# Kernel optimization log

Measured on AMD Instinct MI355X. Metric: run time of the kernel, lower is better.

The kernel has to match this reference:

```python
import jax, jax.numpy as jnp
import numpy as np

N, E, G = 50000, 600000, 50
IN_CH, HID, OUT, HEADS = 5, 64, 32, 4
BN_EPS = 1e-5


def setup_inputs() -> dict:
    key = jax.random.key(0)
    ks = jax.random.split(key, 32)

    def p(i, shape, scale=0.1):
        return jax.random.normal(ks[i], shape, dtype=jnp.float32) * scale

    inp = {
        "x": jax.random.normal(ks[0], (N, IN_CH), dtype=jnp.float32),
        "edge_index": jax.random.randint(ks[1], (2, E), 0, N),
        "batch": jnp.sort(jax.random.randint(ks[2], (N,), 0, G)),
        "enc_w": p(3, (IN_CH, HID)),
        "enc_b": jnp.zeros((HID,), jnp.float32),
    }
    dims = [(HID, HID), (HID, HID), (HID, OUT)]
    i = 4
    for l, (din, dout) in enumerate(dims):
        inp[f"w{l}"] = p(i, (din, HEADS * dout)); i += 1
        inp[f"as{l}"] = p(i, (HEADS, dout)); i += 1
        inp[f"ad{l}"] = p(i, (HEADS, dout)); i += 1
        inp[f"b{l}"] = jnp.zeros((dout,), jnp.float32)
        inp[f"g{l}"] = jnp.ones((dout,), jnp.float32)
        inp[f"be{l}"] = jnp.zeros((dout,), jnp.float32)
    for name in ("eth", "man"):
        inp[f"{name}_w1"] = p(i, (OUT, OUT // 2)); i += 1
        inp[f"{name}_b1"] = jnp.zeros((OUT // 2,), jnp.float32)
        inp[f"{name}_w2"] = p(i, (OUT // 2, 1)); i += 1
        inp[f"{name}_b2"] = jnp.zeros((1,), jnp.float32)
    return inp


def _gat(h_in, src, dst, W, a_s, a_d, bias, dout):
    # PyG GATConv, heads=HEADS, concat=False (mean over heads)
    h = (h_in @ W).reshape(N, HEADS, dout)          # [N,H,C]
    es = (h * a_s).sum(-1)                          # [N,H] src attention term
    ed = (h * a_d).sum(-1)                          # [N,H] dst attention term
    e = jax.nn.leaky_relu(es[src] + ed[dst], 0.2)   # [E,H]
    m = jax.ops.segment_max(e, dst, num_segments=N)
    ex = jnp.exp(e - m[dst])
    s = jax.ops.segment_sum(ex, dst, num_segments=N)
    alpha = ex / (s[dst] + 1e-16)                   # edge softmax per dst
    out = jax.ops.segment_sum(h[src] * alpha[..., None], dst, num_segments=N)
    return out.mean(axis=1) + bias                  # mean over heads + bias


def _bn(x, g, b):  # BatchNorm1d with batch statistics
    mu = x.mean(0)
    var = x.var(0)
    return g * (x - mu) * jax.lax.rsqrt(var + BN_EPS) + b


def _head(g, w1, b1, w2, b2):
    return jax.nn.sigmoid(jax.nn.relu(g @ w1 + b1) @ w2 + b2)


def reference(x, edge_index, batch, enc_w, enc_b,
              w0, as0, ad0, b0, g0, be0,
              w1, as1, ad1, b1, g1, be1,
              w2, as2, ad2, b2, g2, be2,
              eth_w1, eth_b1, eth_w2, eth_b2,
              man_w1, man_b1, man_w2, man_b2):
    loops = jnp.arange(N)
    src = jnp.concatenate([edge_index[0], loops])
    dst = jnp.concatenate([edge_index[1], loops])

    h = x @ enc_w + enc_b
    layers = [(w0, as0, ad0, b0, g0, be0, HID),
              (w1, as1, ad1, b1, g1, be1, HID),
              (w2, as2, ad2, b2, g2, be2, OUT)]
    for i, (W, a_s, a_d, bias, gm, bt, dout) in enumerate(layers):
        h = _gat(h, src, dst, W, a_s, a_d, bias, dout)
        h = _bn(h, gm, bt)
        if i < len(layers) - 1:
            h = jax.nn.relu(h)  # dropout is identity at inference

    ones = jnp.ones((N,), h.dtype)
    counts = jax.ops.segment_sum(ones, batch, num_segments=G)  # [G]
    gsum = jax.ops.segment_sum(h, batch, num_segments=G)
    gmean = gsum / jnp.maximum(counts, 1.0)[:, None]
    gmax = jax.ops.segment_max(h, batch, num_segments=G)
    gmax = jnp.where(counts[:, None] > 0, gmax, 0.0)
    gemb = (gmean + gmax + gsum) / 3.0

    ethics = _head(gemb, eth_w1, eth_b1, eth_w2, eth_b2)
    manip = _head(gemb, man_w1, man_b1, man_w2, man_b2)
    return h, gemb, ethics, manip
```

## Files before the change

### kernel.cpp

```cpp
#include <hip/hip_runtime.h>
#include <math.h>

constexpr int kN  = 50000;
constexpr int kE  = 600000;
constexpr int kET = 650000;
constexpr int kG  = 50;
constexpr int kH  = 4;
constexpr int kRep = 16;
constexpr int kRangeSz = 6250;

constexpr size_t OFF_HCUR   = 0;
constexpr size_t OFF_HNEXT  = 1600000;
constexpr size_t OFF_Z      = 4800000;
constexpr size_t OFF_ES     = 11200000;
constexpr size_t OFF_ED     = 11400000;
constexpr size_t OFF_ROWPTR = 14200000;
constexpr size_t OFF_SRC    = 14320000;
constexpr size_t OFF_WT2    = 14970000;
constexpr size_t OFF_AHAT   = 15000000;
constexpr size_t OFF_SPART  = 15002000;
constexpr size_t OFF_CURSOR = 15010000;
constexpr size_t OFF_BNREP  = 15060000;
constexpr size_t OFF_GPOOL  = 15066144;
constexpr size_t kZeroEnd   = 15069344;

constexpr int kScanBlocks = (kN + 1023) / 1024;
constexpr int kHistBlocks = (kET + 255) / 256;
constexpr int kPrepBlocks = 163;
constexpr int kEncBlocks  = kN / 4;
constexpr int kChunks     = (kE + 1023) / 1024;
constexpr int kSctBlocks  = kChunks * 8;
constexpr int kLoopBlocks = (kN + 255) / 256;

typedef __bf16 bf16x8 __attribute__((ext_vector_type(8)));
typedef float  f32x4  __attribute__((ext_vector_type(4)));

__device__ inline ushort f2b(float f) {
    unsigned u = __float_as_uint(f);
    return (ushort)((u + 0x7FFFu + ((u >> 16) & 1u)) >> 16);
}
__device__ inline float b2f(ushort u) {
    return __uint_as_float(((unsigned)u) << 16);
}
__device__ inline unsigned enc_f(float f) {
    unsigned b = __float_as_uint(f);
    return (b & 0x80000000u) ? ~b : (b | 0x80000000u);
}
__device__ inline float dec_f(unsigned u) {
    return __uint_as_float((u & 0x80000000u) ? (u & 0x7FFFFFFFu) : ~u);
}

__device__ inline void edge_pair(const int* __restrict__ ei, int e, int& src, int& dst) {
    if (e < kE) { src = ei[e]; dst = ei[kE + e]; }
    else        { src = e - kE; dst = e - kE; }
}

__global__ void k_histprep(const int* __restrict__ ei, int* __restrict__ counts,
                           const float* __restrict__ w0, const float* __restrict__ w1,
                           const float* __restrict__ w2, const float* __restrict__ as0,
                           const float* __restrict__ as1, const float* __restrict__ as2,
                           const float* __restrict__ ad0, const float* __restrict__ ad1,
                           const float* __restrict__ ad2, float* __restrict__ ahat,
                           ushort* __restrict__ Wt2) {
    int b = blockIdx.x;
    if (b < 3) {
        const float* W  = (b == 0) ? w0 : (b == 1) ? w1 : w2;
        const float* As = (b == 0) ? as0 : (b == 1) ? as1 : as2;
        const float* Ad = (b == 0) ? ad0 : (b == 1) ? ad1 : ad2;
        int dout = (b == 2) ? 32 : 64;
        int i = threadIdx.x;
        int h = i >> 6, k = i & 63;
        const float* wr = W + (size_t)k * (4 * dout) + h * dout;
        float s1 = 0.f, s2 = 0.f;
        for (int c = 0; c < dout; ++c) {
            float w = wr[c];
            s1 += w * As[h * dout + c];
            s2 += w * Ad[h * dout + c];
        }
        ahat[b * 512 + i] = s1;
        ahat[b * 512 + 256 + i] = s2;
    } else if (b < kPrepBlocks) {
        int i = (b - 3) * 256 + threadIdx.x;
        if (i >= 40960) return;
        int l, li;
        if (i < 16384)      { l = 0; li = i; }
        else if (i < 32768) { l = 1; li = i - 16384; }
        else                { l = 2; li = i - 32768; }
        int dout = (l == 2) ? 32 : 64;
        const float* W = (l == 0) ? w0 : (l == 1) ? w1 : w2;
        int c = li >> 8, kk = li & 255;
        int h = kk >> 6, k = kk & 63;
        Wt2[l * 16384 + li] = f2b(W[(size_t)k * (4 * dout) + h * dout + c]);
    } else {
        int e = (b - kPrepBlocks) * 256 + threadIdx.x;
        if (e >= kET) return;
        int src, dst;
        edge_pair(ei, e, src, dst);
        atomicAdd(&counts[dst], 1);
    }
}

__global__ void __launch_bounds__(1024) k_scan_local(const int* __restrict__ counts,
                                                     int* __restrict__ rowptr,
                                                     int* __restrict__ partials) {
    int tid = threadIdx.x;
    int idx = blockIdx.x * 1024 + tid;
    int val = (idx < kN) ? counts[idx] : 0;
    int lane = tid & 63, w = tid >> 6;
    int x = val;
#pragma unroll
    for (int off = 1; off < 64; off <<= 1) {
        int t = __shfl_up(x, off);
        if (lane >= off) x += t;
    }
    __shared__ int wsum[16];
    if (lane == 63) wsum[w] = x;
    __syncthreads();
    if (w == 0 && lane < 16) {
        int y = wsum[lane];
#pragma unroll
        for (int off = 1; off < 16; off <<= 1) {
            int t = __shfl_up(y, off);
            if (lane >= off) y += t;
        }
        wsum[lane] = y;
    }
    __syncthreads();
    int incl = x + (w > 0 ? wsum[w - 1] : 0);
    if (idx < kN) rowptr[idx + 1] = incl;
    if (tid == 1023) partials[blockIdx.x] = incl;
}

__global__ void k_scan_part(int* __restrict__ partials) {
    int lane = threadIdx.x;
    int v = (lane < kScanBlocks) ? partials[lane] : 0;
    int x = v;
#pragma unroll
    for (int off = 1; off < 64; off <<= 1) {
        int t = __shfl_up(x, off);
        if (lane >= off) x += t;
    }
    if (lane < kScanBlocks) partials[lane] = x - v;
}

__global__ void __launch_bounds__(1024) k_scan_add(int* __restrict__ cursor,
                                                   int* __restrict__ rowptr,
                                                   const int* __restrict__ partials) {
    int idx = blockIdx.x * 1024 + threadIdx.x;
    if (idx >= kN) return;
    int incl = rowptr[idx + 1] + partials[blockIdx.x];
    rowptr[idx + 1] = incl;
    int val = cursor[idx];
    cursor[idx] = incl - val;
    if (idx == 0) rowptr[0] = 0;
}

__global__ void __launch_bounds__(256) k_scatter_enc(const int* __restrict__ ei,
                                                     int* __restrict__ cursor,
                                                     ushort* __restrict__ src_csr,
                                                     const int* __restrict__ rowptr,
                                                     const float* __restrict__ x,
                                                     const float* __restrict__ w,
                                                     const float* __restrict__ b,
                                                     const float* __restrict__ ahat0,
                                                     ushort* __restrict__ h,
                                                     float* __restrict__ es,
                                                     float* __restrict__ ed) {
    if (blockIdx.x < kEncBlocks) {
        int node = blockIdx.x * 4 + (threadIdx.x >> 6);
        int lane = threadIdx.x & 63;
        float acc = b[lane];
#pragma unroll
        for (int k = 0; k < 5; ++k) acc += x[node * 5 + k] * w[k * 64 + lane];
        h[(size_t)node * 64 + lane] = f2b(acc);

        float ps[4], pd[4];
#pragma unroll
        for (int hh = 0; hh < 4; ++hh) {
            ps[hh] = acc * ahat0[hh * 64 + lane];
            pd[hh] = acc * ahat0[256 + hh * 64 + lane];
        }
#pragma unroll
        for (int off = 1; off < 64; off <<= 1) {
#pragma unroll
            for (int hh = 0; hh < 4; ++hh) {
                ps[hh] += __shfl_xor(ps[hh], off);
                pd[hh] += __shfl_xor(pd[hh], off);
            }
        }
        if (lane == 0) {
            ((float4*)es)[node] = make_float4(ps[0], ps[1], ps[2], ps[3]);
            ((float4*)ed)[node] = make_float4(pd[0], pd[1], pd[2], pd[3]);
        }
    } else if (blockIdx.x < kEncBlocks + kSctBlocks) {
        int bs = blockIdx.x - kEncBlocks;
        int chunk = bs >> 3;
        int range = blockIdx.x & 7;
        int dlo = range * kRangeSz;
        int e0 = (chunk * 256 + threadIdx.x) * 4;
        if (e0 >= kE) return;
        int4 dv = *reinterpret_cast<const int4*>(ei + kE + e0);
        int4 sv = *reinterpret_cast<const int4*>(ei + e0);
        int dstv[4] = {dv.x, dv.y, dv.z, dv.w};
        int srcv[4] = {sv.x, sv.y, sv.z, sv.w};
#pragma unroll
        for (int u = 0; u < 4; ++u) {
            if (e0 + u < kE && (unsigned)(dstv[u] - dlo) < (unsigned)kRangeSz) {
                int pos = atomicAdd(&cursor[dstv[u]], 1);
                src_csr[pos] = (ushort)srcv[u];
            }
        }
    } else {
        int d = (blockIdx.x - kEncBlocks - kSctBlocks) * 256 + threadIdx.x;
        if (d >= kN) return;
        src_csr[rowptr[d + 1] - 1] = (ushort)d;
    }
}

__global__ void __launch_bounds__(256) k_gat(const int* __restrict__ rowptr,
                                             const ushort* __restrict__ srcc,
                                             const float* __restrict__ es,
                                             const float* __restrict__ ed,
                                             const ushort* __restrict__ h,
                                             ushort* __restrict__ z) {
    int wid = threadIdx.x >> 6;
    int lane = threadIdx.x & 63;
    int dst = blockIdx.x * 4 + wid;
    int start = rowptr[dst], end = rowptr[dst + 1];
    int deg = end - start;

    int e_l = lane >> 2, hh = lane & 3;
    int q = lane >> 4, c4 = lane & 15;

    float edv = ed[dst * 4 + hh];
    float acc[4][4] = {};
    float s;

    if (deg <= 16) {
        int pos = start + e_l;
        int psafe = (pos < end) ? pos : start;
        int src = srcc[psafe];
        float v = es[src * 4 + hh] + edv;
        v = (v >= 0.f) ? v : 0.2f * v;
        if (pos >= end) v = -3e38f;

        uint2 hv[4];
#pragma unroll
        for (int t = 0; t < 4; ++t) {
            int p2 = start + t * 4 + q;
            int p2s = (p2 < end) ? p2 : start;
            int s2 = srcc[p2s];
            hv[t] = *reinterpret_cast<const uint2*>(h + (size_t)s2 * 64 + c4 * 4);
        }

        float cm = v;
        cm = fmaxf(cm, __shfl_xor(cm, 4));
        cm = fmaxf(cm, __shfl_xor(cm, 8));
        cm = fmaxf(cm, __shfl_xor(cm, 16));
        cm = fmaxf(cm, __shfl_xor(cm, 32));
        float p = __expf(v - cm);
        float cs = p;
        cs += __shfl_xor(cs, 4);
        cs += __shfl_xor(cs, 8);
        cs += __shfl_xor(cs, 16);
        cs += __shfl_xor(cs, 32);
        s = cs;

#pragma unroll
        for (int t = 0; t < 4; ++t) {
            int el = t * 4 + q;
            float p0 = __shfl(p, (el << 2) | 0);
            float p1 = __shfl(p, (el << 2) | 1);
            float p2 = __shfl(p, (el << 2) | 2);
            float p3 = __shfl(p, (el << 2) | 3);
            float c0 = __uint_as_float(hv[t].x << 16);
            float c1 = __uint_as_float(hv[t].x & 0xFFFF0000u);
            float c2 = __uint_as_float(hv[t].y << 16);
            float c3 = __uint_as_float(hv[t].y & 0xFFFF0000u);
            acc[0][0] += p0 * c0; acc[0][1] += p0 * c1; acc[0][2] += p0 * c2; acc[0][3] += p0 * c3;
            acc[1][0] += p1 * c0; acc[1][1] += p1 * c1; acc[1][2] += p1 * c2; acc[1][3] += p1 * c3;
            acc[2][0] += p2 * c0; acc[2][1] += p2 * c1; acc[2][2] += p2 * c2; acc[2][3] += p2 * c3;
            acc[3][0] += p3 * c0; acc[3][1] += p3 * c1; acc[3][2] += p3 * c2; acc[3][3] += p3 * c3;
        }
    } else {
        float m = -3e38f;
        s = 0.f;
        for (int cs0 = start; cs0 < end; cs0 += 16) {
            int pos = cs0 + e_l;
            int psafe = (pos < end) ? pos : start;
            int src = srcc[psafe];
            float v = es[src * 4 + hh] + edv;
            v = (v >= 0.f) ? v : 0.2f * v;
            if (pos >= end) v = -3e38f;

            float cm = v;
            cm = fmaxf(cm, __shfl_xor(cm, 4));
            cm = fmaxf(cm, __shfl_xor(cm, 8));
            cm = fmaxf(cm, __shfl_xor(cm, 16));
            cm = fmaxf(cm, __shfl_xor(cm, 32));
            float mn = fmaxf(m, cm);
            float scale = __expf(m - mn);
            float p = __expf(v - mn);
            float cth = p;
            cth += __shfl_xor(cth, 4);
            cth += __shfl_xor(cth, 8);
            cth += __shfl_xor(cth, 16);
            cth += __shfl_xor(cth, 32);
            s = s * scale + cth;
            m = mn;

            float sc0 = __shfl(scale, 0), sc1 = __shfl(scale, 1);
            float sc2 = __shfl(scale, 2), sc3 = __shfl(scale, 3);
#pragma unroll
            for (int c = 0; c < 4; ++c) {
                acc[0][c] *= sc0; acc[1][c] *= sc1; acc[2][c] *= sc2; acc[3][c] *= sc3;
            }
#pragma unroll
            for (int t = 0; t < 4; ++t) {
                int el = t * 4 + q;
                int p2 = cs0 + el;
                int p2s = (p2 < end) ? p2 : start;
                int s2 = srcc[p2s];
                uint2 hv = *reinterpret_cast<const uint2*>(h + (size_t)s2 * 64 + c4 * 4);
                float p0 = __shfl(p, (el << 2) | 0);
                float p1 = __shfl(p, (el << 2) | 1);
                float p2f = __shfl(p, (el << 2) | 2);
                float p3 = __shfl(p, (el << 2) | 3);
                float c0 = __uint_as_float(hv.x << 16);
                float c1 = __uint_as_float(hv.x & 0xFFFF0000u);
                float c2 = __uint_as_float(hv.y << 16);
                float c3 = __uint_as_float(hv.y & 0xFFFF0000u);
                acc[0][0] += p0 * c0;  acc[0][1] += p0 * c1;  acc[0][2] += p0 * c2;  acc[0][3] += p0 * c3;
                acc[1][0] += p1 * c0;  acc[1][1] += p1 * c1;  acc[1][2] += p1 * c2;  acc[1][3] += p1 * c3;
                acc[2][0] += p2f * c0; acc[2][1] += p2f * c1; acc[2][2] += p2f * c2; acc[2][3] += p2f * c3;
                acc[3][0] += p3 * c0;  acc[3][1] += p3 * c1;  acc[3][2] += p3 * c2;  acc[3][3] += p3 * c3;
            }
        }
    }

    float myinv = 0.25f / (s + 1e-16f);
    float inv0 = __shfl(myinv, 0), inv1 = __shfl(myinv, 1);
    float inv2 = __shfl(myinv, 2), inv3 = __shfl(myinv, 3);
#pragma unroll
    for (int c = 0; c < 4; ++c) {
        acc[0][c] *= inv0; acc[1][c] *= inv1; acc[2][c] *= inv2; acc[3][c] *= inv3;
    }
#pragma unroll
    for (int j = 0; j < 4; ++j) {
#pragma unroll
        for (int c = 0; c < 4; ++c) {
            float v = acc[j][c];
            v += __shfl_xor(v, 16);
            v += __shfl_xor(v, 32);
            acc[j][c] = v;
        }
    }
    if (q == 0) {
        ushort* zr = z + (size_t)dst * 256 + c4 * 4;
#pragma unroll
        for (int j = 0; j < 4; ++j) {
            ushort4 o;
            o.x = f2b(acc[j][0]); o.y = f2b(acc[j][1]);
            o.z = f2b(acc[j][2]); o.w = f2b(acc[j][3]);
            *reinterpret_cast<ushort4*>(zr + j * 64) = o;
        }
    }
}

template <int DOUT>
__global__ void __launch_bounds__(256) k_zgemm(const ushort* __restrict__ z,
                                               const ushort* __restrict__ Wt2l,
                                               float* __restrict__ hnext,
                                               float* __restrict__ bnrep_l) {
    constexpr int NT = DOUT / 16;
    constexpr int W = 2 * DOUT;
    __shared__ float pl[4][W];
    int tid = threadIdx.x;
    int widx = tid >> 6, lane = tid & 63;
    int wid = blockIdx.x * 4 + widx;
    int mtile = wid / NT;
    int nt = wid - mtile * NT;
    bool active = (mtile < kN / 16);
    int m0 = mtile * 16;
    int n0 = nt * 16;

    int row = lane & 15;
    int k0  = (lane >> 4) * 8;

    for (int j = tid; j < 4 * W; j += 256) (&pl[0][0])[j] = 0.f;

    f32x4 acc = {0.f, 0.f, 0.f, 0.f};
    if (active) {
        const ushort* za = z + (size_t)(m0 + row) * 256 + k0;
        const ushort* wb = Wt2l + (size_t)(n0 + row) * 256 + k0;
#pragma unroll
        for (int ks = 0; ks < 8; ++ks) {
            bf16x8 a = *reinterpret_cast<const bf16x8*>(za + ks * 32);
            bf16x8 b = *reinterpret_cast<const bf16x8*>(wb + ks * 32);
            acc = __builtin_amdgcn_mfma_f32_16x16x32_bf16(a, b, acc, 0, 0, 0);
        }
        int col = lane & 15;
        int r0  = (lane >> 4) * 4;
#pragma unroll
        for (int r = 0; r < 4; ++r)
            hnext[(size_t)(m0 + r0 + r) * DOUT + n0 + col] = acc[r];
    }

    float s0 = 0.f, q0 = 0.f;
#pragma unroll
    for (int r = 0; r < 4; ++r) { s0 += acc[r]; q0 += acc[r] * acc[r]; }
    s0 += __shfl_xor(s0, 16); s0 += __shfl_xor(s0, 32);
    q0 += __shfl_xor(q0, 16); q0 += __shfl_xor(q0, 32);
    __syncthreads();
    if (lane < 16) {
        pl[widx][n0 + lane]        = s0;
        pl[widx][DOUT + n0 + lane] = q0;
    }
    __syncthreads();
    if (tid < W) {
        float t = pl[0][tid] + pl[1][tid] + pl[2][tid] + pl[3][tid];
        atomicAdd(&bnrep_l[(blockIdx.x & (kRep - 1)) * 128 + tid], t);
    }
}

__global__ void __launch_bounds__(256) k_bn_apply_att(const float* __restrict__ hnext,
                                                      const float* __restrict__ bnrep_l,
                                                      const float* __restrict__ g,
                                                      const float* __restrict__ be,
                                                      const float* __restrict__ ahat_next,
                                                      ushort* __restrict__ hcur,
                                                      float* __restrict__ es,
                                                      float* __restrict__ ed) {
    int node = blockIdx.x * 4 + (threadIdx.x >> 6);
    int lane = threadIdx.x & 63;
    float bs = 0.f, bq = 0.f;
#pragma unroll
    for (int r = 0; r < kRep; ++r) {
        bs += bnrep_l[r * 128 + lane];
        bq += bnrep_l[r * 128 + 64 + lane];
    }
    float mu = bs * (1.f / kN);
    float var = bq * (1.f / kN) - mu * mu;
    float v = g[lane] * (hnext[(size_t)node * 64 + lane] - mu) * rsqrtf(var + 1e-5f) + be[lane];
    v = fmaxf(v, 0.f);
    hcur[(size_t)node * 64 + lane] = f2b(v);

    float ps[4], pd[4];
#pragma unroll
    for (int hh = 0; hh < 4; ++hh) {
        ps[hh] = v * ahat_next[hh * 64 + lane];
        pd[hh] = v * ahat_next[256 + hh * 64 + lane];
    }
#pragma unroll
    for (int off = 1; off < 64; off <<= 1) {
#pragma unroll
        for (int hh = 0; hh < 4; ++hh) {
            ps[hh] += __shfl_xor(ps[hh], off);
            pd[hh] += __shfl_xor(pd[hh], off);
        }
    }
    if (lane == 0) {
        ((float4*)es)[node] = make_float4(ps[0], ps[1], ps[2], ps[3]);
        ((float4*)ed)[node] = make_float4(pd[0], pd[1], pd[2], pd[3]);
    }
}

__global__ void __launch_bounds__(256) k_bn_apply32_pool(const float* __restrict__ hnext,
                                                         const float* __restrict__ bnrep_l,
                                                         const float* __restrict__ g,
                                                         const float* __restrict__ be,
                                                         const int* __restrict__ batch,
                                                         float* __restrict__ out_h,
                                                         float* __restrict__ gsum,
                                                         unsigned* __restrict__ gmaxe) {
    int tid = threadIdx.x;
    int i = blockIdx.x * 256 + tid;
    int n = i >> 5, c = i & 31;
    float bs = 0.f, bq = 0.f;
#pragma unroll
    for (int r = 0; r < kRep; ++r) {
        bs += bnrep_l[r * 128 + c];
        bq += bnrep_l[r * 128 + 32 + c];
    }
    float mu = bs * (1.f / kN);
    float var = bq * (1.f / kN) - mu * mu;
    float v = g[c] * (hnext[i] - mu) * rsqrtf(var + 1e-5f) + be[c];
    out_h[i] = v;

    __shared__ float ls[256];
    ls[tid] = v;
    __syncthreads();
    int nb0 = blockIdx.x * 8;
    int gfirst = batch[nb0], glast = batch[nb0 + 7];
    if (gfirst == glast) {
        if (tid < 32) {
            float s = 0.f;
            unsigned me = 0u;
#pragma unroll
            for (int r = 0; r < 8; ++r) {
                float vv = ls[r * 32 + tid];
                s += vv;
                unsigned e = enc_f(vv);
                me = (e > me) ? e : me;
            }
            atomicAdd(&gsum[gfirst * 32 + tid], s);
            atomicMax(&gmaxe[gfirst * 32 + tid], me);
        }
    } else {
        int gg = batch[n];
        atomicAdd(&gsum[gg * 32 + c], v);
        atomicMax(&gmaxe[gg * 32 + c], enc_f(v));
    }
}

__global__ void __launch_bounds__(256) k_finish(const float* __restrict__ gsum,
                                                const unsigned* __restrict__ gmaxe,
                                                const int* __restrict__ batch,
                                                const float* __restrict__ ew1,
                                                const float* __restrict__ eb1,
                                                const float* __restrict__ ew2,
                                                const float* __restrict__ eb2,
                                                const float* __restrict__ mw1,
                                                const float* __restrict__ mb1,
                                                const float* __restrict__ mw2,
                                                const float* __restrict__ mb2,
                                                float* __restrict__ out_gemb,
                                                float* __restrict__ out_eth,
                                                float* __restrict__ out_man) {
    __shared__ int bound[kG + 1];
    __shared__ float ge[kG * 32];
    int tid = threadIdx.x;
    if (tid <= kG) {
        int lo = 0, hi = kN;
        while (lo < hi) { int mid = (lo + hi) >> 1; if (batch[mid] < tid) lo = mid + 1; else hi = mid; }
        bound[tid] = lo;
    }
    __syncthreads();
    for (int j = tid; j < kG * 32; j += 256) {
        int gg = j >> 5;
        int cnt = bound[gg + 1] - bound[gg];
        float sum = gsum[j];
        float mx = (cnt > 0) ? dec_f(gmaxe[j]) : 0.f;
        float mean = sum / fmaxf((float)cnt, 1.f);
        float e = (mean + mx + sum) * (1.f / 3.f);
        ge[j] = e;
        out_gemb[j] = e;
    }
    __syncthreads();
    if (tid < kG) {
        const float* row = &ge[tid * 32];
        float acc_e = eb2[0], acc_m = mb2[0];
#pragma unroll 4
        for (int j = 0; j < 16; ++j) {
            float he = eb1[j], hm = mb1[j];
            for (int k = 0; k < 32; ++k) {
                float v = row[k];
                he += v * ew1[k * 16 + j];
                hm += v * mw1[k * 16 + j];
            }
            acc_e += fmaxf(he, 0.f) * ew2[j];
            acc_m += fmaxf(hm, 0.f) * mw2[j];
        }
        out_eth[tid] = 1.f / (1.f + expf(-acc_e));
        out_man[tid] = 1.f / (1.f + expf(-acc_m));
    }
}

extern "C" void kernel_launch(void* const* d_in, const int* in_sizes, int n_in,
                              void* d_out, int out_size, void* d_ws, size_t ws_size,
                              hipStream_t stream) {
    const float* x     = (const float*)d_in[0];
    const int*   ei    = (const int*)d_in[1];
    const int*   batch = (const int*)d_in[2];
    const float* enc_w = (const float*)d_in[3];
    const float* enc_b = (const float*)d_in[4];

    float* ws = (float*)d_ws;
    ushort*   hcur  = (ushort*)(ws + OFF_HCUR);
    float*    hnext = ws + OFF_HNEXT;
    ushort*   z     = (ushort*)(ws + OFF_Z);
    float*    es    = ws + OFF_ES;
    float*    ed    = ws + OFF_ED;
    int*      rowptr= (int*)(ws + OFF_ROWPTR);
    ushort*   srcc  = (ushort*)(ws + OFF_SRC);
    ushort*   Wt2   = (ushort*)(ws + OFF_WT2);
    float*    ahat  = ws + OFF_AHAT;
    int*      spart = (int*)(ws + OFF_SPART);
    int*      cursor= (int*)(ws + OFF_CURSOR);
    float*    bnrep = ws + OFF_BNREP;
    float*    gsum  = ws + OFF_GPOOL;
    unsigned* gmaxe = (unsigned*)(ws + OFF_GPOOL + 1600);

    float* out      = (float*)d_out;
    float* out_h    = out;
    float* out_gemb = out + 1600000;
    float* out_eth  = out + 1601600;
    float* out_man  = out + 1601650;

    hipMemsetAsync(ws + OFF_CURSOR, 0, (kZeroEnd - OFF_CURSOR) * sizeof(float), stream);

    k_histprep<<<kPrepBlocks + kHistBlocks, 256, 0, stream>>>(
        ei, cursor,
        (const float*)d_in[5], (const float*)d_in[11], (const float*)d_in[17],
        (const float*)d_in[6], (const float*)d_in[12], (const float*)d_in[18],
        (const float*)d_in[7], (const float*)d_in[13], (const float*)d_in[19],
        ahat, Wt2);

    k_scan_local<<<kScanBlocks, 1024, 0, stream>>>(cursor, rowptr, spart);
    k_scan_part<<<1, 64, 0, stream>>>(spart);
    k_scan_add<<<kScanBlocks, 1024, 0, stream>>>(cursor, rowptr, spart);

    k_scatter_enc<<<kEncBlocks + kSctBlocks + kLoopBlocks, 256, 0, stream>>>(
        ei, cursor, srcc, rowptr, x, enc_w, enc_b, ahat, hcur, es, ed);

    for (int l = 0; l < 3; ++l) {
        const float* gam = (const float*)d_in[9 + 6 * l];
        const float* bet = (const float*)d_in[10 + 6 * l];
        const ushort* Wt2l = Wt2 + l * 16384;
        float* bnrep_l = bnrep + l * kRep * 128;

        k_gat<<<kN / 4, 256, 0, stream>>>(rowptr, srcc, es, ed, hcur, z);

        if (l < 2) {
            k_zgemm<64><<<3125, 256, 0, stream>>>(z, Wt2l, hnext, bnrep_l);
            k_bn_apply_att<<<kN / 4, 256, 0, stream>>>(hnext, bnrep_l, gam, bet,
                                                       ahat + (l + 1) * 512, hcur, es, ed);
        } else {
            k_zgemm<32><<<1563, 256, 0, stream>>>(z, Wt2l, hnext, bnrep_l);
            k_bn_apply32_pool<<<kN * 32 / 256, 256, 0, stream>>>(hnext, bnrep_l, gam, bet,
                                                                 batch, out_h, gsum, gmaxe);
        }
    }

    k_finish<<<1, 256, 0, stream>>>(gsum, gmaxe, batch,
                                    (const float*)d_in[23], (const float*)d_in[24],
                                    (const float*)d_in[25], (const float*)d_in[26],
                                    (const float*)d_in[27], (const float*)d_in[28],
                                    (const float*)d_in[29], (const float*)d_in[30],
                                    out_gemb, out_eth, out_man);
}
```

Measured before the change: 473.7 us.

## Restructure GAT aggregation to one channel per lane with LDS-shared attention weights

The GAT aggregation kernel drops its separate low-degree path and its cross-quarter shuffle reduction. Each lane now owns one of the 64 channels and loops serially over the edges in a chunk. Softmax weights and rescale factors are passed through per-wave shared memory instead of shuffles. This removes many shuffles and the final reduction, but gathers of h become 2-byte scalar loads done one edge at a time. That means more sequential memory latency per destination, and the shared-memory exchange relies on the wave running in lockstep with no barrier.

```diff
diff --git a/kernel.cpp b/kernel.cpp
--- a/kernel.cpp
+++ b/kernel.cpp
@@ -223,148 +223,70 @@
                                              const float* __restrict__ ed,
                                              const ushort* __restrict__ h,
                                              ushort* __restrict__ z) {
+    __shared__ float pls[4][72];
     int wid = threadIdx.x >> 6;
     int lane = threadIdx.x & 63;
     int dst = blockIdx.x * 4 + wid;
     int start = rowptr[dst], end = rowptr[dst + 1];
-    int deg = end - start;
 
     int e_l = lane >> 2, hh = lane & 3;
-    int q = lane >> 4, c4 = lane & 15;
+    int c = lane;
 
     float edv = ed[dst * 4 + hh];
-    float acc[4][4] = {};
-    float s;
-
-    if (deg <= 16) {
-        int pos = start + e_l;
+    float acc0 = 0.f, acc1 = 0.f, acc2 = 0.f, acc3 = 0.f;
+    float m = -3e38f, s = 0.f;
+    float* pw = pls[wid];
+
+    for (int cs0 = start; cs0 < end; cs0 += 16) {
+        int pos = cs0 + e_l;
         int psafe = (pos < end) ? pos : start;
         int src = srcc[psafe];
         float v = es[src * 4 + hh] + edv;
         v = (v >= 0.f) ? v : 0.2f * v;
         if (pos >= end) v = -3e38f;
 
-        uint2 hv[4];
-#pragma unroll
-        for (int t = 0; t < 4; ++t) {
-            int p2 = start + t * 4 + q;
-            int p2s = (p2 < end) ? p2 : start;
-            int s2 = srcc[p2s];
-            hv[t] = *reinterpret_cast<const uint2*>(h + (size_t)s2 * 64 + c4 * 4);
-        }
-
         float cm = v;
         cm = fmaxf(cm, __shfl_xor(cm, 4));
         cm = fmaxf(cm, __shfl_xor(cm, 8));
         cm = fmaxf(cm, __shfl_xor(cm, 16));
         cm = fmaxf(cm, __shfl_xor(cm, 32));
-        float p = __expf(v - cm);
-        float cs = p;
-        cs += __shfl_xor(cs, 4);
-        cs += __shfl_xor(cs, 8);
-        cs += __shfl_xor(cs, 16);
-        cs += __shfl_xor(cs, 32);
-        s = cs;
-
-#pragma unroll
-        for (int t = 0; t < 4; ++t) {
-            int el = t * 4 + q;
-            float p0 = __shfl(p, (el << 2) | 0);
-            float p1 = __shfl(p, (el << 2) | 1);
-            float p2 = __shfl(p, (el << 2) | 2);
-            float p3 = __shfl(p, (el << 2) | 3);
-            float c0 = __uint_as_float(hv[t].x << 16);
-            float c1 = __uint_as_float(hv[t].x & 0xFFFF0000u);
-            float c2 = __uint_as_float(hv[t].y << 16);
-            float c3 = __uint_as_float(hv[t].y & 0xFFFF0000u);
-            acc[0][0] += p0 * c0; acc[0][1] += p0 * c1; acc[0][2] += p0 * c2; acc[0][3] += p0 * c3;
-            acc[1][0] += p1 * c0; acc[1][1] += p1 * c1; acc[1][2] += p1 * c2; acc[1][3] += p1 * c3;
-            acc[2][0] += p2 * c0; acc[2][1] += p2 * c1; acc[2][2] += p2 * c2; acc[2][3] += p2 * c3;
-            acc[3][0] += p3 * c0; acc[3][1] += p3 * c1; acc[3][2] += p3 * c2; acc[3][3] += p3 * c3;
-        }
-    } else {
-        float m = -3e38f;
-        s = 0.f;
-        for (int cs0 = start; cs0 < end; cs0 += 16) {
-            int pos = cs0 + e_l;
-            int psafe = (pos < end) ? pos : start;
-            int src = srcc[psafe];
-            float v = es[src * 4 + hh] + edv;
-            v = (v >= 0.f) ? v : 0.2f * v;
-            if (pos >= end) v = -3e38f;
-
-            float cm = v;
-            cm = fmaxf(cm, __shfl_xor(cm, 4));
-            cm = fmaxf(cm, __shfl_xor(cm, 8));
-            cm = fmaxf(cm, __shfl_xor(cm, 16));
-            cm = fmaxf(cm, __shfl_xor(cm, 32));
-            float mn = fmaxf(m, cm);
-            float scale = __expf(m - mn);
-            float p = __expf(v - mn);
-            float cth = p;
-            cth += __shfl_xor(cth, 4);
-            cth += __shfl_xor(cth, 8);
-            cth += __shfl_xor(cth, 16);
-            cth += __shfl_xor(cth, 32);
-            s = s * scale + cth;
-            m = mn;
-
-            float sc0 = __shfl(scale, 0), sc1 = __shfl(scale, 1);
-            float sc2 = __shfl(scale, 2), sc3 = __shfl(scale, 3);
-#pragma unroll
-            for (int c = 0; c < 4; ++c) {
-                acc[0][c] *= sc0; acc[1][c] *= sc1; acc[2][c] *= sc2; acc[3][c] *= sc3;
-            }
-#pragma unroll
-            for (int t = 0; t < 4; ++t) {
-                int el = t * 4 + q;
-                int p2 = cs0 + el;
-                int p2s = (p2 < end) ? p2 : start;
-                int s2 = srcc[p2s];
-                uint2 hv = *reinterpret_cast<const uint2*>(h + (size_t)s2 * 64 + c4 * 4);
-                float p0 = __shfl(p, (el << 2) | 0);
-                float p1 = __shfl(p, (el << 2) | 1);
-                float p2f = __shfl(p, (el << 2) | 2);
-                float p3 = __shfl(p, (el << 2) | 3);
-                float c0 = __uint_as_float(hv.x << 16);
-                float c1 = __uint_as_float(hv.x & 0xFFFF0000u);
-                float c2 = __uint_as_float(hv.y << 16);
-                float c3 = __uint_as_float(hv.y & 0xFFFF0000u);
-                acc[0][0] += p0 * c0;  acc[0][1] += p0 * c1;  acc[0][2] += p0 * c2;  acc[0][3] += p0 * c3;
-                acc[1][0] += p1 * c0;  acc[1][1] += p1 * c1;  acc[1][2] += p1 * c2;  acc[1][3] += p1 * c3;
-                acc[2][0] += p2f * c0; acc[2][1] += p2f * c1; acc[2][2] += p2f * c2; acc[2][3] += p2f * c3;
-                acc[3][0] += p3 * c0;  acc[3][1] += p3 * c1;  acc[3][2] += p3 * c2;  acc[3][3] += p3 * c3;
-            }
-        }
-    }
-
-    float myinv = 0.25f / (s + 1e-16f);
-    float inv0 = __shfl(myinv, 0), inv1 = __shfl(myinv, 1);
-    float inv2 = __shfl(myinv, 2), inv3 = __shfl(myinv, 3);
-#pragma unroll
-    for (int c = 0; c < 4; ++c) {
-        acc[0][c] *= inv0; acc[1][c] *= inv1; acc[2][c] *= inv2; acc[3][c] *= inv3;
-    }
-#pragma unroll
-    for (int j = 0; j < 4; ++j) {
-#pragma unroll
-        for (int c = 0; c < 4; ++c) {
-            float v = acc[j][c];
-            v += __shfl_xor(v, 16);
-            v += __shfl_xor(v, 32);
-            acc[j][c] = v;
-        }
-    }
-    if (q == 0) {
-        ushort* zr = z + (size_t)dst * 256 + c4 * 4;
-#pragma unroll
-        for (int j = 0; j < 4; ++j) {
-            ushort4 o;
-            o.x = f2b(acc[j][0]); o.y = f2b(acc[j][1]);
-            o.z = f2b(acc[j][2]); o.w = f2b(acc[j][3]);
-            *reinterpret_cast<ushort4*>(zr + j * 64) = o;
-        }
-    }
+        float mn = fmaxf(m, cm);
+        float scale = __expf(m - mn);
+        float p = __expf(v - mn);
+        float cth = p;
+        cth += __shfl_xor(cth, 4);
+        cth += __shfl_xor(cth, 8);
+        cth += __shfl_xor(cth, 16);
+        cth += __shfl_xor(cth, 32);
+        s = s * scale + cth;
+        m = mn;
+
+        pw[lane] = p;
+        if (lane < 4) pw[64 + lane] = scale;
+        float4 scv = *reinterpret_cast<const float4*>(&pw[64]);
+        acc0 *= scv.x; acc1 *= scv.y; acc2 *= scv.z; acc3 *= scv.w;
+
+        int nedge = min(end - cs0, 16);
+#pragma unroll 4
+        for (int e = 0; e < nedge; ++e) {
+            int srcE = srcc[cs0 + e];
+            float4 pe = *reinterpret_cast<const float4*>(&pw[e * 4]);
+            float hc = b2f(h[(size_t)srcE * 64 + c]);
+            acc0 += pe.x * hc;
+            acc1 += pe.y * hc;
+            acc2 += pe.z * hc;
+            acc3 += pe.w * hc;
+        }
+    }
+
+    if (lane < 4) pw[64 + lane] = 0.25f / (s + 1e-16f);
+    float4 iv = *reinterpret_cast<const float4*>(&pw[64]);
+
+    ushort* zr = z + (size_t)dst * 256 + c;
+    zr[0]   = f2b(acc0 * iv.x);
+    zr[64]  = f2b(acc1 * iv.y);
+    zr[128] = f2b(acc2 * iv.z);
+    zr[192] = f2b(acc3 * iv.w);
 }
 
 template <int DOUT>
```

Measured after the change: 473.0 us. About the same (-0.1%).
